# Kernel optimization log

Measured on AMD Instinct MI355X. Metric: run time of the kernel, lower is better.

Reference implementation:

```python
import jax, jax.numpy as jnp
import numpy as np

NEG_SLOPE = 0.01  # torch LeakyReLU default

def leaky_relu(x):
    return jnp.where(x >= 0, x, NEG_SLOPE * x)

def setup_inputs() -> dict:
    key = jax.random.key(0)
    ks = jax.random.split(key, 12)
    D = 128
    N_U, N_I, E = 100000, 50000, 1000000
    s = 1.0 / np.sqrt(D)
    return {
        "h_user": jax.random.normal(ks[0], (N_U, D), jnp.float32),
        "h_item": jax.random.normal(ks[1], (N_I, D), jnp.float32),
        "src_idx": jax.random.randint(ks[2], (E,), 0, N_U, jnp.int64) if jax.config.jax_enable_x64 else jax.random.randint(ks[2], (E,), 0, N_U, jnp.int32),
        "dst_idx": jax.random.randint(ks[3], (E,), 0, N_I, jnp.int32),
        "W_left": jax.random.normal(ks[4], (D, D), jnp.float32) * s,
        "b_left": jax.random.normal(ks[5], (D,), jnp.float32) * s,
        "W_right": jax.random.normal(ks[6], (D, D), jnp.float32) * s,
        "b_right": jax.random.normal(ks[7], (D,), jnp.float32) * s,
        "W1": jax.random.normal(ks[8], (D, D), jnp.float32) * s,
        "b1": jax.random.normal(ks[9], (D,), jnp.float32) * s,
        "W2": jax.random.normal(ks[10], (D, 1), jnp.float32) * s,
        "b2": jax.random.normal(ks[11], (1,), jnp.float32) * s,
    }

def reference(h_user, h_item, src_idx, dst_idx,
              W_left, b_left, W_right, b_right, W1, b1, W2, b2):
    # node linear transforms (dropout is identity in eval mode)
    u_f = h_user @ W_left + b_left      # [N_u, D]
    i_f = h_item @ W_right + b_right    # [N_i, D]
    # edge gather + add (dgl fn.u_add_v)
    score = u_f[src_idx] + i_f[dst_idx]  # [E, D]
    # pred MLP: LeakyReLU -> Linear(D,D) -> LeakyReLU -> Linear(D,1) -> LeakyReLU
    x = leaky_relu(score)
    x = leaky_relu(x @ W1 + b1)
    x = leaky_relu(x @ W2 + b2)         # [E, 1]
    return x
```

## Files before the change

### kernel.cpp

```cpp
#include <hip/hip_runtime.h>

typedef __attribute__((ext_vector_type(8))) short bf16x8;
typedef __attribute__((ext_vector_type(4))) float f32x4;

__device__ __forceinline__ float leaky(float v) { return fmaxf(v, 0.01f * v); }

__device__ __forceinline__ float bf2f(short s) {
    return __uint_as_float(((unsigned int)(unsigned short)s) << 16);
}

__device__ __forceinline__ unsigned short f2bf(float a) {
    unsigned int u = __float_as_uint(a);
    return (unsigned short)((u + 0x7FFFu + ((u >> 16) & 1u)) >> 16);
}

__device__ __forceinline__ unsigned int pk_bf16(float a, float b) {
    unsigned int ua = __float_as_uint(a);
    ua = (ua + 0x7FFFu + ((ua >> 16) & 1u)) >> 16;
    unsigned int ub = __float_as_uint(b);
    ub = (ub + 0x7FFFu + ((ub >> 16) & 1u)) >> 16;
    return ua | (ub << 16);
}

__global__ __launch_bounds__(128) void prep(const float* __restrict__ WL,
                                            const float* __restrict__ WR,
                                            const float* __restrict__ W1,
                                            unsigned short* __restrict__ WLf,
                                            unsigned short* __restrict__ WRf,
                                            unsigned short* __restrict__ Wf) {
    int g = blockIdx.x;
    int f = (g & 127) * 128 + threadIdx.x;
    int j = f & 7, lane = (f >> 3) & 63, nt = (f >> 9) & 7, kb = f >> 12;
    int n = nt * 16 + (lane & 15);
    int kf = kb * 32 + (lane >> 4) * 8 + j;
    if (g < 128) {
        WLf[f] = f2bf(WL[kf * 128 + n]);
    } else if (g < 256) {
        WRf[f] = f2bf(WR[kf * 128 + n]);
    } else {
        int k = (kf & 7) * 16 + (kf >> 3);
        Wf[f] = f2bf(W1[k * 128 + n]);
    }
}

#define PITCH 136

__global__ __launch_bounds__(256, 4) void node_mfma2(const float* __restrict__ h_user,
                                                     const float* __restrict__ h_item,
                                                     const unsigned short* __restrict__ WLf,
                                                     const unsigned short* __restrict__ WRf,
                                                     const float* __restrict__ b_left,
                                                     const float* __restrict__ b_right,
                                                     unsigned short* __restrict__ u_f,
                                                     unsigned short* __restrict__ i_f,
                                                     int N_U, int N_I, int BU) {
    bool isU = (int)blockIdx.x < BU;
    const float* h = isU ? h_user : h_item;
    const unsigned short* Wfr = isU ? WLf : WRf;
    const float* b = isU ? b_left : b_right;
    unsigned short* out = isU ? u_f : i_f;
    int N = isU ? N_U : N_I;
    int r0 = (isU ? blockIdx.x : blockIdx.x - BU) * 128;

    __shared__ unsigned short xt[128 * PITCH];
    int t = threadIdx.x;
    int s = t & 15;
    int el0 = t >> 4;
#pragma unroll
    for (int pass = 0; pass < 8; ++pass) {
        int el = pass * 16 + el0;
        int row = min(r0 + el, N - 1);
        const f32x4* hp = (const f32x4*)(h + (size_t)row * 128);
        f32x4 a0 = hp[s];
        f32x4 a1 = hp[s + 16];
        unsigned int* rp = (unsigned int*)(xt + el * PITCH);
        rp[2 * s]          = pk_bf16(a0.x, a0.y);
        rp[2 * s + 1]      = pk_bf16(a0.z, a0.w);
        rp[32 + 2 * s]     = pk_bf16(a1.x, a1.y);
        rp[32 + 2 * s + 1] = pk_bf16(a1.z, a1.w);
    }
    __syncthreads();

    int wave = t >> 6;
    int lane = t & 63;
    int m0 = wave * 32;
    int col = lane & 15;
    int quad = lane >> 4;

    f32x4 acc[2][8];
#pragma unroll
    for (int mt = 0; mt < 2; ++mt)
#pragma unroll
        for (int nt = 0; nt < 8; ++nt) acc[mt][nt] = (f32x4){0.f, 0.f, 0.f, 0.f};

#pragma unroll
    for (int kb = 0; kb < 4; ++kb) {
        bf16x8 afr[2];
#pragma unroll
        for (int mt = 0; mt < 2; ++mt)
            afr[mt] = *(const bf16x8*)(xt + (m0 + mt * 16 + col) * PITCH + kb * 32 + quad * 8);
#pragma unroll
        for (int nt = 0; nt < 8; ++nt) {
            bf16x8 bfr = *(const bf16x8*)(Wfr + ((kb * 8 + nt) * 64 + lane) * 8);
            acc[0][nt] = __builtin_amdgcn_mfma_f32_16x16x32_bf16(afr[0], bfr, acc[0][nt], 0, 0, 0);
            acc[1][nt] = __builtin_amdgcn_mfma_f32_16x16x32_bf16(afr[1], bfr, acc[1][nt], 0, 0, 0);
        }
    }

#pragma unroll
    for (int mt = 0; mt < 2; ++mt)
#pragma unroll
        for (int rr = 0; rr < 4; ++rr) {
            int row = r0 + m0 + mt * 16 + quad * 4 + rr;
            bf16x8 v;
#pragma unroll
            for (int nt = 0; nt < 8; ++nt)
                v[nt] = (short)f2bf(acc[mt][nt][rr] + b[nt * 16 + col]);
            if (row < N) *(bf16x8*)(out + (size_t)row * 128 + col * 8) = v;
        }
}

#define TE 128

__global__ __launch_bounds__(512, 8) void edge_kernel(
    const unsigned short* __restrict__ u_f, const unsigned short* __restrict__ i_f,
    const int* __restrict__ src, const int* __restrict__ dst,
    const unsigned short* __restrict__ Wf,
    const float* __restrict__ b1, const float* __restrict__ W2,
    const float* __restrict__ b2, float* __restrict__ out, int E) {
    __shared__ unsigned short xt[TE * PITCH];
    __shared__ float zb[4][2][32];
    int t = threadIdx.x;
    int e0 = blockIdx.x * TE;

    int s = t & 15;
    int el0 = t >> 4;
#pragma unroll
    for (int pass = 0; pass < 4; ++pass) {
        int el = pass * 32 + el0;
        int ec = min(e0 + el, E - 1);
        bf16x8 u8 = *(const bf16x8*)(u_f + (size_t)src[ec] * 128 + s * 8);
        bf16x8 i8 = *(const bf16x8*)(i_f + (size_t)dst[ec] * 128 + s * 8);
        bf16x8 a;
#pragma unroll
        for (int j = 0; j < 8; j += 2) {
            float x0 = leaky(bf2f(u8[j])     + bf2f(i8[j]));
            float x1 = leaky(bf2f(u8[j + 1]) + bf2f(i8[j + 1]));
            unsigned int p = pk_bf16(x0, x1);
            a[j]     = (short)(p & 0xFFFFu);
            a[j + 1] = (short)(p >> 16);
        }
        *(bf16x8*)(xt + el * PITCH + s * 8) = a;
    }
    __syncthreads();

    int wave = t >> 6;
    int lane = t & 63;
    int col = lane & 15;
    int quad = lane >> 4;
    int wp = wave >> 1;
    int ch = wave & 1;
    int m0 = wp * 32;

    f32x4 acc[2][4];
#pragma unroll
    for (int mt = 0; mt < 2; ++mt)
#pragma unroll
        for (int i = 0; i < 4; ++i) acc[mt][i] = (f32x4){0.f, 0.f, 0.f, 0.f};

#pragma unroll
    for (int kb = 0; kb < 4; ++kb) {
        bf16x8 afr[2];
#pragma unroll
        for (int mt = 0; mt < 2; ++mt)
            afr[mt] = *(const bf16x8*)(xt + (m0 + mt * 16 + col) * PITCH + kb * 32 + quad * 8);
#pragma unroll
        for (int i = 0; i < 4; ++i) {
            int nt = ch * 4 + i;
            bf16x8 bfr = *(const bf16x8*)(Wf + ((kb * 8 + nt) * 64 + lane) * 8);
            acc[0][i] = __builtin_amdgcn_mfma_f32_16x16x32_bf16(afr[0], bfr, acc[0][i], 0, 0, 0);
            acc[1][i] = __builtin_amdgcn_mfma_f32_16x16x32_bf16(afr[1], bfr, acc[1][i], 0, 0, 0);
        }
    }

    float p[2][4];
#pragma unroll
    for (int mt = 0; mt < 2; ++mt)
#pragma unroll
        for (int rr = 0; rr < 4; ++rr) p[mt][rr] = 0.f;

#pragma unroll
    for (int i = 0; i < 4; ++i) {
        int n = (ch * 4 + i) * 16 + col;
        float bb = b1[n];
        float ww = W2[n];
#pragma unroll
        for (int mt = 0; mt < 2; ++mt)
#pragma unroll
            for (int rr = 0; rr < 4; ++rr) p[mt][rr] += leaky(acc[mt][i][rr] + bb) * ww;
    }
#pragma unroll
    for (int off = 1; off < 16; off <<= 1)
#pragma unroll
        for (int mt = 0; mt < 2; ++mt)
#pragma unroll
            for (int rr = 0; rr < 4; ++rr) p[mt][rr] += __shfl_xor(p[mt][rr], off, 64);

    if (col == 0) {
#pragma unroll
        for (int mt = 0; mt < 2; ++mt)
#pragma unroll
            for (int rr = 0; rr < 4; ++rr)
                zb[wp][ch][mt * 16 + quad * 4 + rr] = p[mt][rr];
    }
    __syncthreads();

    if (t < 128) {
        int g = t >> 5;
        int idx = t & 31;
        float z = zb[g][0][idx] + zb[g][1][idx] + b2[0];
        int e = e0 + g * 32 + idx;
        if (e < E) out[e] = leaky(z);
    }
}

extern "C" void kernel_launch(void* const* d_in, const int* in_sizes, int n_in,
                              void* d_out, int out_size, void* d_ws, size_t ws_size,
                              hipStream_t stream) {
    const float* h_user  = (const float*)d_in[0];
    const float* h_item  = (const float*)d_in[1];
    const int*   src_idx = (const int*)d_in[2];
    const int*   dst_idx = (const int*)d_in[3];
    const float* W_left  = (const float*)d_in[4];
    const float* b_left  = (const float*)d_in[5];
    const float* W_right = (const float*)d_in[6];
    const float* b_right = (const float*)d_in[7];
    const float* W1      = (const float*)d_in[8];
    const float* b1      = (const float*)d_in[9];
    const float* W2      = (const float*)d_in[10];
    const float* b2      = (const float*)d_in[11];
    float* out = (float*)d_out;

    int N_U = in_sizes[0] / 128;
    int N_I = in_sizes[1] / 128;
    int E   = in_sizes[2];

    unsigned short* Wf  = (unsigned short*)d_ws;
    unsigned short* WLf = Wf + 16384;
    unsigned short* WRf = WLf + 16384;
    unsigned short* u_f = (unsigned short*)((char*)d_ws + 131072);
    unsigned short* i_f = u_f + (size_t)N_U * 128;

    prep<<<384, 128, 0, stream>>>(W_left, W_right, W1, WLf, WRf, Wf);

    int BU = (N_U + 127) / 128;
    int BI = (N_I + 127) / 128;
    node_mfma2<<<BU + BI, 256, 0, stream>>>(h_user, h_item, WLf, WRf, b_left, b_right,
                                            u_f, i_f, N_U, N_I, BU);

    edge_kernel<<<(E + TE - 1) / TE, 512, 0, stream>>>(u_f, i_f, src_idx, dst_idx,
                                                       Wf, b1, W2, b2, out, E);
}
```

Measured before the change: 233.0 us.

## Double edge tile size and use hardware bf16 packing with packed float math

The edge kernel now handles 256 edges per block instead of 128. Each wave pair covers 64 rows with four M tiles, so every W1 fragment loaded from global memory is reused across more MFMAs. Float-to-bf16 conversion uses the hardware cvt_pk_bf16 builtin when it is available, and the unpack, LeakyReLU and bias epilogues are written as packed 2- and 4-wide vector ops to cut ALU instructions. The larger tile doubles LDS and accumulator registers and lowers the occupancy target to 4 blocks, which may reduce latency hiding for the random gathers.

```diff
diff --git a/kernel.cpp b/kernel.cpp
--- a/kernel.cpp
+++ b/kernel.cpp
@@ -2,24 +2,34 @@
 
 typedef __attribute__((ext_vector_type(8))) short bf16x8;
 typedef __attribute__((ext_vector_type(4))) float f32x4;
+typedef __attribute__((ext_vector_type(2))) float f32x2;
 
 __device__ __forceinline__ float leaky(float v) { return fmaxf(v, 0.01f * v); }
-
-__device__ __forceinline__ float bf2f(short s) {
-    return __uint_as_float(((unsigned int)(unsigned short)s) << 16);
-}
 
 __device__ __forceinline__ unsigned short f2bf(float a) {
     unsigned int u = __float_as_uint(a);
     return (unsigned short)((u + 0x7FFFu + ((u >> 16) & 1u)) >> 16);
 }
 
-__device__ __forceinline__ unsigned int pk_bf16(float a, float b) {
+__device__ __forceinline__ unsigned int cvtpk(float a, float b) {
+#if __has_builtin(__builtin_amdgcn_cvt_pk_bf16_f32)
+    typedef __attribute__((ext_vector_type(2))) __bf16 bf2_t;
+    bf2_t v = __builtin_amdgcn_cvt_pk_bf16_f32(a, b);
+    return __builtin_bit_cast(unsigned int, v);
+#else
     unsigned int ua = __float_as_uint(a);
     ua = (ua + 0x7FFFu + ((ua >> 16) & 1u)) >> 16;
     unsigned int ub = __float_as_uint(b);
     ub = (ub + 0x7FFFu + ((ub >> 16) & 1u)) >> 16;
     return ua | (ub << 16);
+#endif
+}
+
+__device__ __forceinline__ f32x2 unpk2(unsigned int d) {
+    f32x2 r;
+    r.x = __uint_as_float(d << 16);
+    r.y = __uint_as_float(d & 0xFFFF0000u);
+    return r;
 }
 
 __global__ __launch_bounds__(128) void prep(const float* __restrict__ WL,
@@ -74,10 +84,10 @@
         f32x4 a0 = hp[s];
         f32x4 a1 = hp[s + 16];
         unsigned int* rp = (unsigned int*)(xt + el * PITCH);
-        rp[2 * s]          = pk_bf16(a0.x, a0.y);
-        rp[2 * s + 1]      = pk_bf16(a0.z, a0.w);
-        rp[32 + 2 * s]     = pk_bf16(a1.x, a1.y);
-        rp[32 + 2 * s + 1] = pk_bf16(a1.z, a1.w);
+        rp[2 * s]          = cvtpk(a0.x, a0.y);
+        rp[2 * s + 1]      = cvtpk(a0.z, a0.w);
+        rp[32 + 2 * s]     = cvtpk(a1.x, a1.y);
+        rp[32 + 2 * s + 1] = cvtpk(a1.z, a1.w);
     }
     __syncthreads();
 
@@ -107,50 +117,61 @@
         }
     }
 
+    float bb[8];
+#pragma unroll
+    for (int nt = 0; nt < 8; ++nt) bb[nt] = b[nt * 16 + col];
 #pragma unroll
     for (int mt = 0; mt < 2; ++mt)
 #pragma unroll
         for (int rr = 0; rr < 4; ++rr) {
             int row = r0 + m0 + mt * 16 + quad * 4 + rr;
-            bf16x8 v;
-#pragma unroll
-            for (int nt = 0; nt < 8; ++nt)
-                v[nt] = (short)f2bf(acc[mt][nt][rr] + b[nt * 16 + col]);
-            if (row < N) *(bf16x8*)(out + (size_t)row * 128 + col * 8) = v;
-        }
-}
-
-#define TE 128
-
-__global__ __launch_bounds__(512, 8) void edge_kernel(
+            uint4 v;
+            v.x = cvtpk(acc[mt][0][rr] + bb[0], acc[mt][1][rr] + bb[1]);
+            v.y = cvtpk(acc[mt][2][rr] + bb[2], acc[mt][3][rr] + bb[3]);
+            v.z = cvtpk(acc[mt][4][rr] + bb[4], acc[mt][5][rr] + bb[5]);
+            v.w = cvtpk(acc[mt][6][rr] + bb[6], acc[mt][7][rr] + bb[7]);
+            if (row < N) *(uint4*)(out + (size_t)row * 128 + col * 8) = v;
+        }
+}
+
+#define TE 256
+
+__global__ __launch_bounds__(512, 4) void edge_kernel(
     const unsigned short* __restrict__ u_f, const unsigned short* __restrict__ i_f,
     const int* __restrict__ src, const int* __restrict__ dst,
     const unsigned short* __restrict__ Wf,
     const float* __restrict__ b1, const float* __restrict__ W2,
     const float* __restrict__ b2, float* __restrict__ out, int E) {
     __shared__ unsigned short xt[TE * PITCH];
-    __shared__ float zb[4][2][32];
+    __shared__ float zb[4][2][64];
     int t = threadIdx.x;
     int e0 = blockIdx.x * TE;
 
     int s = t & 15;
     int el0 = t >> 4;
 #pragma unroll
-    for (int pass = 0; pass < 4; ++pass) {
+    for (int pass = 0; pass < 8; ++pass) {
         int el = pass * 32 + el0;
         int ec = min(e0 + el, E - 1);
-        bf16x8 u8 = *(const bf16x8*)(u_f + (size_t)src[ec] * 128 + s * 8);
-        bf16x8 i8 = *(const bf16x8*)(i_f + (size_t)dst[ec] * 128 + s * 8);
-        bf16x8 a;
-#pragma unroll
-        for (int j = 0; j < 8; j += 2) {
-            float x0 = leaky(bf2f(u8[j])     + bf2f(i8[j]));
-            float x1 = leaky(bf2f(u8[j + 1]) + bf2f(i8[j + 1]));
-            unsigned int p = pk_bf16(x0, x1);
-            a[j]     = (short)(p & 0xFFFFu);
-            a[j + 1] = (short)(p >> 16);
-        }
-        *(bf16x8*)(xt + el * PITCH + s * 8) = a;
+        uint4 u4 = *(const uint4*)(u_f + (size_t)src[ec] * 128 + s * 8);
+        uint4 i4 = *(const uint4*)(i_f + (size_t)dst[ec] * 128 + s * 8);
+        uint4 a;
+        {
+            f32x2 v;
+            v = unpk2(u4.x) + unpk2(i4.x);
+            v = __builtin_elementwise_max(v, v * 0.01f);
+            a.x = cvtpk(v.x, v.y);
+            v = unpk2(u4.y) + unpk2(i4.y);
+            v = __builtin_elementwise_max(v, v * 0.01f);
+            a.y = cvtpk(v.x, v.y);
+            v = unpk2(u4.z) + unpk2(i4.z);
+            v = __builtin_elementwise_max(v, v * 0.01f);
+            a.z = cvtpk(v.x, v.y);
+            v = unpk2(u4.w) + unpk2(i4.w);
+            v = __builtin_elementwise_max(v, v * 0.01f);
+            a.w = cvtpk(v.x, v.y);
+        }
+        *(uint4*)(xt + el * PITCH + s * 8) = a;
     }
     __syncthreads();
 
@@ -160,34 +181,33 @@
     int quad = lane >> 4;
     int wp = wave >> 1;
     int ch = wave & 1;
-    int m0 = wp * 32;
-
-    f32x4 acc[2][4];
-#pragma unroll
-    for (int mt = 0; mt < 2; ++mt)
+    int m0 = wp * 64;
+
+    f32x4 acc[4][4];
+#pragma unroll
+    for (int mt = 0; mt < 4; ++mt)
 #pragma unroll
         for (int i = 0; i < 4; ++i) acc[mt][i] = (f32x4){0.f, 0.f, 0.f, 0.f};
 
 #pragma unroll
     for (int kb = 0; kb < 4; ++kb) {
-        bf16x8 afr[2];
-#pragma unroll
-        for (int mt = 0; mt < 2; ++mt)
+        bf16x8 afr[4];
+#pragma unroll
+        for (int mt = 0; mt < 4; ++mt)
             afr[mt] = *(const bf16x8*)(xt + (m0 + mt * 16 + col) * PITCH + kb * 32 + quad * 8);
 #pragma unroll
         for (int i = 0; i < 4; ++i) {
             int nt = ch * 4 + i;
             bf16x8 bfr = *(const bf16x8*)(Wf + ((kb * 8 + nt) * 64 + lane) * 8);
-            acc[0][i] = __builtin_amdgcn_mfma_f32_16x16x32_bf16(afr[0], bfr, acc[0][i], 0, 0, 0);
-            acc[1][i] = __builtin_amdgcn_mfma_f32_16x16x32_bf16(afr[1], bfr, acc[1][i], 0, 0, 0);
-        }
-    }
-
-    float p[2][4];
-#pragma unroll
-    for (int mt = 0; mt < 2; ++mt)
-#pragma unroll
-        for (int rr = 0; rr < 4; ++rr) p[mt][rr] = 0.f;
+#pragma unroll
+            for (int mt = 0; mt < 4; ++mt)
+                acc[mt][i] = __builtin_amdgcn_mfma_f32_16x16x32_bf16(afr[mt], bfr, acc[mt][i], 0, 0, 0);
+        }
+    }
+
+    f32x4 p[4];
+#pragma unroll
+    for (int mt = 0; mt < 4; ++mt) p[mt] = (f32x4){0.f, 0.f, 0.f, 0.f};
 
 #pragma unroll
     for (int i = 0; i < 4; ++i) {
@@ -195,31 +215,33 @@
         float bb = b1[n];
         float ww = W2[n];
 #pragma unroll
-        for (int mt = 0; mt < 2; ++mt)
-#pragma unroll
-            for (int rr = 0; rr < 4; ++rr) p[mt][rr] += leaky(acc[mt][i][rr] + bb) * ww;
+        for (int mt = 0; mt < 4; ++mt) {
+            f32x4 y = acc[mt][i] + bb;
+            y = __builtin_elementwise_max(y, y * 0.01f);
+            p[mt] += y * ww;
+        }
     }
 #pragma unroll
     for (int off = 1; off < 16; off <<= 1)
 #pragma unroll
-        for (int mt = 0; mt < 2; ++mt)
+        for (int mt = 0; mt < 4; ++mt)
 #pragma unroll
             for (int rr = 0; rr < 4; ++rr) p[mt][rr] += __shfl_xor(p[mt][rr], off, 64);
 
     if (col == 0) {
 #pragma unroll
-        for (int mt = 0; mt < 2; ++mt)
+        for (int mt = 0; mt < 4; ++mt)
 #pragma unroll
             for (int rr = 0; rr < 4; ++rr)
                 zb[wp][ch][mt * 16 + quad * 4 + rr] = p[mt][rr];
     }
     __syncthreads();
 
-    if (t < 128) {
-        int g = t >> 5;
-        int idx = t & 31;
+    if (t < 256) {
+        int g = t >> 6;
+        int idx = t & 63;
         float z = zb[g][0][idx] + zb[g][1][idx] + b2[0];
-        int e = e0 + g * 32 + idx;
+        int e = e0 + g * 64 + idx;
         if (e < E) out[e] = leaky(z);
     }
 }
```

Measured after the change: 233.8 us. About the same (+0.4%).
